# Performance work log

Hardware: AMD Instinct MI355X
Metric: run time of the kernel (lower is better)

The kernel has to match this reference:

```python
import jax, jax.numpy as jnp
import numpy as np

OUTPUT_SIZE = (32, 32, 32)
TRUNCATION = (24, 24, 24)


def dct_matrix(N):
    # Orthonormal DCT-II matrix M with y_k = sum_n M[k, n] * x_n.
    n = jnp.arange(N, dtype=jnp.float32)
    k = n[:, None]
    M = jnp.cos(jnp.pi * (n[None, :] + 0.5) * k / N)
    scale = jnp.where(n == 0, jnp.sqrt(1.0 / N), jnp.sqrt(2.0 / N))
    return M * scale[:, None]


def setup_inputs() -> dict:
    key = jax.random.key(0)
    x = jax.random.normal(key, (4, 64, 64, 64, 32), dtype=jnp.float32)
    return {"x": x}


def reference(x) -> jnp.ndarray:
    # x: [B, D, H, W, C]
    B, D, H, W, C = x.shape
    t0, t1, t2 = TRUNCATION
    o0, o1, o2 = OUTPUT_SIZE

    # 3D DCT-II (ortho), separable per spatial axis.
    Md, Mh, Mw = dct_matrix(D), dct_matrix(H), dct_matrix(W)
    y = jnp.einsum('pd,bdhwc->bphwc', Md, x)
    y = jnp.einsum('qh,bphwc->bpqwc', Mh, y)
    y = jnp.einsum('rw,bpqwc->bpqrc', Mw, y)

    # Crop low frequencies, zero-pad to output size.
    y = y[:, :t0, :t1, :t2, :]
    y = jnp.pad(y, ((0, 0), (0, o0 - t0), (0, o1 - t1), (0, o2 - t2), (0, 0)))

    # 3D inverse DCT (ortho inverse = transpose of DCT matrix).
    I0, I1, I2 = dct_matrix(o0).T, dct_matrix(o1).T, dct_matrix(o2).T
    z = jnp.einsum('dp,bpqrc->bdqrc', I0, y)
    z = jnp.einsum('hq,bdqrc->bdhrc', I1, z)
    z = jnp.einsum('wr,bdhrc->bdhwc', I2, z)

    # Original module's _idct3D permutes (0,4,3,2,1) then back, which reverses
    # the spatial axis order of the output: out[b, w, h, d, c].
    return jnp.transpose(z, (0, 3, 2, 1, 4))
```

## Files before the change

kernel.cpp:

```cpp
#include <hip/hip_runtime.h>


#define PI_D 3.14159265358979323846

__global__ __launch_bounds__(256) void sp_compute_A(float* __restrict__ A) {
    int idx = blockIdx.x * 256 + threadIdx.x;
    if (idx >= 2048) return;
    int o = idx >> 6;
    int i = idx & 63;
    double acc = 0.0;
    for (int p = 0; p < 24; ++p) {
        double s32 = (p == 0) ? sqrt(1.0 / 32.0) : sqrt(2.0 / 32.0);
        double s64 = (p == 0) ? sqrt(1.0 / 64.0) : sqrt(2.0 / 64.0);
        acc += s32 * cos(PI_D * (o + 0.5) * p / 32.0)
             * s64 * cos(PI_D * (i + 0.5) * p / 64.0);
    }
    A[idx] = (float)acc;
}

__global__ __launch_bounds__(256) void sp_contract(
        const float* __restrict__ X, const float* __restrict__ Amat,
        float* __restrict__ Y, int N) {
    __shared__ float As[64][32];
    int t = threadIdx.x;
    for (int i = t; i < 2048; i += 256) {
        int p = i >> 6, k = i & 63;
        As[k][p] = Amat[i];
    }
    __syncthreads();

    long b  = blockIdx.y;
    long n2 = (long)blockIdx.x * 256 + t;
    long s2 = (long)(N >> 1);

    const float2* xp = (const float2*)X + b * 64 * s2 + n2;

    float2 acc[32];
#pragma unroll
    for (int p = 0; p < 32; ++p) acc[p] = make_float2(0.f, 0.f);

    for (int k = 0; k < 64; ++k) {
        float2 xv = xp[(long)k * s2];
        const float4* Arow = (const float4*)&As[k][0];
#pragma unroll
        for (int pg = 0; pg < 8; ++pg) {
            float4 a4 = Arow[pg];
            acc[pg * 4 + 0].x += a4.x * xv.x; acc[pg * 4 + 0].y += a4.x * xv.y;
            acc[pg * 4 + 1].x += a4.y * xv.x; acc[pg * 4 + 1].y += a4.y * xv.y;
            acc[pg * 4 + 2].x += a4.z * xv.x; acc[pg * 4 + 2].y += a4.z * xv.y;
            acc[pg * 4 + 3].x += a4.w * xv.x; acc[pg * 4 + 3].y += a4.w * xv.y;
        }
    }

    float2* yp = (float2*)Y + b * 32 * s2 + n2;
#pragma unroll
    for (int p = 0; p < 32; ++p) yp[(long)p * s2] = acc[p];
}

__global__ __launch_bounds__(256) void sp_contract_w_transpose(
        const float* __restrict__ Y2, const float* __restrict__ Amat,
        float* __restrict__ Out) {
    __shared__ float As[64][32];
    int t = threadIdx.x;
    for (int i = t; i < 2048; i += 256) {
        int r = i >> 6, w = i & 63;
        As[w][r] = Amat[i];
    }
    __syncthreads();

    int j = blockIdx.x * 8 + (t >> 5);
    int c = t & 31;
    int b = j >> 10;
    int p = (j >> 5) & 31;
    int q = j & 31;

    const float* src = Y2 + (long)j * 2048 + c;

    float acc[32];
#pragma unroll
    for (int r = 0; r < 32; ++r) acc[r] = 0.f;

    for (int w = 0; w < 64; ++w) {
        float xv = src[w * 32];
        const float4* Arow = (const float4*)&As[w][0];
#pragma unroll
        for (int rg = 0; rg < 8; ++rg) {
            float4 a4 = Arow[rg];
            acc[rg * 4 + 0] += a4.x * xv;
            acc[rg * 4 + 1] += a4.y * xv;
            acc[rg * 4 + 2] += a4.z * xv;
            acc[rg * 4 + 3] += a4.w * xv;
        }
    }

    float* dst = Out + ((long)(b * 1024 + q)) * 1024 + p * 32 + c;
#pragma unroll
    for (int r = 0; r < 32; ++r) {
        dst[(long)r * 32768] = acc[r];
    }
}

extern "C" void kernel_launch(void* const* d_in, const int* in_sizes, int n_in,
                              void* d_out, int out_size, void* d_ws, size_t ws_size,
                              hipStream_t stream) {
    const float* x = (const float*)d_in[0];
    float* out = (float*)d_out;

    float* A  = (float*)d_ws;
    float* y1 = A + 2048;
    float* y2 = y1 + 16777216;

    sp_compute_A<<<8, 256, 0, stream>>>(A);

    sp_contract<<<dim3(256, 4), 256, 0, stream>>>(x, A, y1, 131072);

    sp_contract<<<dim3(4, 128), 256, 0, stream>>>(y1, A, y2, 2048);

    sp_contract_w_transpose<<<512, 256, 0, stream>>>(y2, A, out);
}
```

Baseline: 273.4 us.

## Reorder DCT pass axes and stage contiguous per-wave tiles via global_load_lds

Replaces the three contraction kernels with one templated per-wave kernel. Each wave loads a 64x32 input tile straight into LDS with global_load_lds, then contracts it against the precomputed 32x64 matrix, using 8 float2 accumulators per thread instead of 32. The contraction order changes to W first, then H, then D, with the output transpose folded into the last pass's store addressing. The aim is fewer registers per thread, better occupancy and coalesced tile loads, at the cost of more LDS per block and a full vmcnt wait before compute with no overlap.

```diff
diff --git a/kernel.cpp b/kernel.cpp
--- a/kernel.cpp
+++ b/kernel.cpp
@@ -18,85 +18,80 @@
     A[idx] = (float)acc;
 }
 
-__global__ __launch_bounds__(256) void sp_contract(
-        const float* __restrict__ X, const float* __restrict__ Amat,
-        float* __restrict__ Y, int N) {
-    __shared__ float As[64][32];
+template<int PASS>
+__global__ __launch_bounds__(256) void sp_pass(const float* __restrict__ X,
+                                               const float* __restrict__ Amat,
+                                               float* __restrict__ Y) {
+    __shared__ float As[2048];
+    __shared__ float tiles[4][2048];
+
     int t = threadIdx.x;
     for (int i = t; i < 2048; i += 256) {
-        int p = i >> 6, k = i & 63;
-        As[k][p] = Amat[i];
+        int k = i >> 5, o = i & 31;
+        As[i] = Amat[o * 64 + k];
     }
     __syncthreads();
 
-    long b  = blockIdx.y;
-    long n2 = (long)blockIdx.x * 256 + t;
-    long s2 = (long)(N >> 1);
+    int wave = t >> 6, lane = t & 63;
+    long tile = (long)blockIdx.x * 4 + wave;
 
-    const float2* xp = (const float2*)X + b * 64 * s2 + n2;
+    constexpr int KS = (PASS == 1) ? 32 : (PASS == 2) ? 1024 : 32768;
+    constexpr int OS = (PASS == 1) ? 32 : (PASS == 2) ? 1024 : 32;
 
-    float2 acc[32];
-#pragma unroll
-    for (int p = 0; p < 32; ++p) acc[p] = make_float2(0.f, 0.f);
-
-    for (int k = 0; k < 64; ++k) {
-        float2 xv = xp[(long)k * s2];
-        const float4* Arow = (const float4*)&As[k][0];
-#pragma unroll
-        for (int pg = 0; pg < 8; ++pg) {
-            float4 a4 = Arow[pg];
-            acc[pg * 4 + 0].x += a4.x * xv.x; acc[pg * 4 + 0].y += a4.x * xv.y;
-            acc[pg * 4 + 1].x += a4.y * xv.x; acc[pg * 4 + 1].y += a4.y * xv.y;
-            acc[pg * 4 + 2].x += a4.z * xv.x; acc[pg * 4 + 2].y += a4.z * xv.y;
-            acc[pg * 4 + 3].x += a4.w * xv.x; acc[pg * 4 + 3].y += a4.w * xv.y;
-        }
+    long in_base, out_base;
+    if constexpr (PASS == 1) {
+        in_base  = tile * 2048;
+        out_base = tile * 1024;
+    } else if constexpr (PASS == 2) {
+        long bd = tile >> 5; int jt = (int)tile & 31;
+        in_base  = bd * 65536 + jt * 32;
+        out_base = bd * 32768 + jt * 32;
+    } else {
+        long b = tile >> 10; int q = ((int)tile >> 5) & 31, r = (int)tile & 31;
+        in_base  = b * 2097152 + q * 1024 + r * 32;
+        out_base = b * 1048576 + r * 32768 + q * 1024;
     }
 
-    float2* yp = (float2*)Y + b * 32 * s2 + n2;
+    float* ltile = &tiles[wave][0];
+    const float* gsrc = X + in_base + (long)(lane >> 3) * KS + (lane & 7) * 4;
 #pragma unroll
-    for (int p = 0; p < 32; ++p) yp[(long)p * s2] = acc[p];
-}
+    for (int i = 0; i < 8; ++i) {
+        __builtin_amdgcn_global_load_lds(
+            (const __attribute__((address_space(1))) void*)(gsrc + (long)i * 8 * KS),
+            (__attribute__((address_space(3))) void*)(ltile + i * 256),
+            16, 0, 0);
+    }
+    asm volatile("s_waitcnt vmcnt(0)" ::: "memory");
+    __builtin_amdgcn_sched_barrier(0);
 
-__global__ __launch_bounds__(256) void sp_contract_w_transpose(
-        const float* __restrict__ Y2, const float* __restrict__ Amat,
-        float* __restrict__ Out) {
-    __shared__ float As[64][32];
-    int t = threadIdx.x;
-    for (int i = t; i < 2048; i += 256) {
-        int r = i >> 6, w = i & 63;
-        As[w][r] = Amat[i];
-    }
-    __syncthreads();
+    int j2 = lane & 15, og = lane >> 4;
+    const float2* xs  = (const float2*)ltile + j2;
+    const float4* as4 = (const float4*)As + og * 2;
 
-    int j = blockIdx.x * 8 + (t >> 5);
-    int c = t & 31;
-    int b = j >> 10;
-    int p = (j >> 5) & 31;
-    int q = j & 31;
+    float2 acc[8];
+#pragma unroll
+    for (int i = 0; i < 8; ++i) acc[i] = make_float2(0.f, 0.f);
 
-    const float* src = Y2 + (long)j * 2048 + c;
-
-    float acc[32];
 #pragma unroll
-    for (int r = 0; r < 32; ++r) acc[r] = 0.f;
-
-    for (int w = 0; w < 64; ++w) {
-        float xv = src[w * 32];
-        const float4* Arow = (const float4*)&As[w][0];
-#pragma unroll
-        for (int rg = 0; rg < 8; ++rg) {
-            float4 a4 = Arow[rg];
-            acc[rg * 4 + 0] += a4.x * xv;
-            acc[rg * 4 + 1] += a4.y * xv;
-            acc[rg * 4 + 2] += a4.z * xv;
-            acc[rg * 4 + 3] += a4.w * xv;
-        }
+    for (int k = 0; k < 64; ++k) {
+        float2 xv = xs[k * 16];
+        float4 a0 = as4[k * 8];
+        float4 a1 = as4[k * 8 + 1];
+        acc[0].x += a0.x * xv.x; acc[0].y += a0.x * xv.y;
+        acc[1].x += a0.y * xv.x; acc[1].y += a0.y * xv.y;
+        acc[2].x += a0.z * xv.x; acc[2].y += a0.z * xv.y;
+        acc[3].x += a0.w * xv.x; acc[3].y += a0.w * xv.y;
+        acc[4].x += a1.x * xv.x; acc[4].y += a1.x * xv.y;
+        acc[5].x += a1.y * xv.x; acc[5].y += a1.y * xv.y;
+        acc[6].x += a1.z * xv.x; acc[6].y += a1.z * xv.y;
+        acc[7].x += a1.w * xv.x; acc[7].y += a1.w * xv.y;
     }
 
-    float* dst = Out + ((long)(b * 1024 + q)) * 1024 + p * 32 + c;
+    float2* dst = (float2*)(Y + out_base) + j2;
 #pragma unroll
-    for (int r = 0; r < 32; ++r) {
-        dst[(long)r * 32768] = acc[r];
+    for (int i = 0; i < 8; ++i) {
+        int o = og * 8 + i;
+        dst[(long)o * (OS / 2)] = acc[i];
     }
 }
 
@@ -112,9 +107,9 @@
 
     sp_compute_A<<<8, 256, 0, stream>>>(A);
 
-    sp_contract<<<dim3(256, 4), 256, 0, stream>>>(x, A, y1, 131072);
+    sp_pass<1><<<4096, 256, 0, stream>>>(x, A, y1);
 
-    sp_contract<<<dim3(4, 128), 256, 0, stream>>>(y1, A, y2, 2048);
+    sp_pass<2><<<2048, 256, 0, stream>>>(y1, A, y2);
 
-    sp_contract_w_transpose<<<512, 256, 0, stream>>>(y2, A, out);
+    sp_pass<3><<<1024, 256, 0, stream>>>(y2, A, out);
 }
```

Result: faster. 253.4 us (-7.3%).
